# Kernel optimization log

Hardware: AMD Instinct MI355X
Metric: run time of the kernel (lower is better)

The kernel has to match this reference:

```python
import jax, jax.numpy as jnp
import numpy as np
from jax import lax

S, B, H, V = 1024, 32, 512, 32000  # seq_len, batch, hidden, vocab


def setup_inputs() -> dict:
    key = jax.random.key(0)
    ks = jax.random.split(key, 12)
    d = {"word_inputs": jax.random.randint(ks[0], (S, B), 0, V)}
    d["embedding"] = jax.random.normal(ks[1], (V, H), jnp.float32) * 0.02
    s = 1.0 / np.sqrt(H)
    i = 2
    for n in ["fwd1", "fwd2", "bwd1", "bwd2"]:
        d[f"W_ih_{n}"] = jax.random.uniform(ks[i], (4 * H, H), jnp.float32, -s, s); i += 1
        d[f"W_hh_{n}"] = jax.random.uniform(ks[i], (4 * H, H), jnp.float32, -s, s); i += 1
        d[f"b_ih_{n}"] = jnp.zeros((4 * H,), jnp.float32)
        d[f"b_hh_{n}"] = jnp.zeros((4 * H,), jnp.float32)
    return d


def _lstm_step(x, h, c, W_ih, W_hh, b, mask):
    # torch.nn.LSTMCell gate order: i, f, g, o
    g = x @ W_ih.T + h @ W_hh.T + b  # [B, 4H]
    i_, f_, g_, o_ = jnp.split(g, 4, axis=-1)
    c_new = jax.nn.sigmoid(f_) * c + jax.nn.sigmoid(i_) * jnp.tanh(g_)
    h_new = jax.nn.sigmoid(o_) * jnp.tanh(c_new)
    m = mask[:, None]  # mask True => keep old state (padding step)
    return jnp.where(m, h, h_new), jnp.where(m, c, c_new)


def _run_direction(emb, masks, p1, p2):
    z = jnp.zeros((emb.shape[1], p1[0].shape[0] // 4), emb.dtype)

    def step(carry, xm):
        h1, c1, h2, c2 = carry
        x, m = xm
        h1, c1 = _lstm_step(x, h1, c1, p1[0], p1[1], p1[2], m)
        h2, c2 = _lstm_step(h1, h2, c2, p2[0], p2[1], p2[2], m)
        return (h1, c1, h2, c2), h2

    carry, hs = lax.scan(step, (z, z, z, z), (emb, masks))
    return hs, carry


def reference(word_inputs, embedding,
              W_ih_fwd1, W_hh_fwd1, b_ih_fwd1, b_hh_fwd1,
              W_ih_fwd2, W_hh_fwd2, b_ih_fwd2, b_hh_fwd2,
              W_ih_bwd1, W_hh_bwd1, b_ih_bwd1, b_hh_bwd1,
              W_ih_bwd2, W_hh_bwd2, b_ih_bwd2, b_hh_bwd2):
    # dropout in eval mode (identity) for a deterministic reference
    emb = embedding[word_inputs]           # [S, B, H]
    masks = word_inputs == 1               # padding token id == 1
    p_f1 = (W_ih_fwd1, W_hh_fwd1, b_ih_fwd1 + b_hh_fwd1)
    p_f2 = (W_ih_fwd2, W_hh_fwd2, b_ih_fwd2 + b_hh_fwd2)
    p_b1 = (W_ih_bwd1, W_hh_bwd1, b_ih_bwd1 + b_hh_bwd1)
    p_b2 = (W_ih_bwd2, W_hh_bwd2, b_ih_bwd2 + b_hh_bwd2)
    fhs, _ = _run_direction(emb, masks, p_f1, p_f2)
    bhs, bcarry = _run_direction(emb[::-1], masks[::-1], p_b1, p_b2)
    # original: outputs[i] = fhs[i] + reversed(bhs)[i] / 2  (note: only bwd halved)
    outputs = fhs + bhs[::-1] / 2
    bh1, bc1, bh2, bc2 = bcarry  # final backward states (bstatus1, bstatus2)
    return outputs, bh1, bc1, bh2, bc2
```

## Files before the change

### kernel.cpp

```cpp
#include <hip/hip_runtime.h>
#include <math.h>


#define SEQ 1024
#define NB 32
#define NH 512
#define BH (NB*NH)
#define NV 32000
#define KP 1032

typedef __attribute__((ext_vector_type(8))) short short8;
typedef __attribute__((ext_vector_type(4))) float f32x4;
typedef unsigned long long u64;

struct P {
  const int*   word;
  const float* emb;
  const float* Wih[4];
  const float* Whh[4];
  const float* bih[4];
  const float* bhh[4];
  unsigned* flags;
  unsigned* gen;
  unsigned short* hpk;
  const unsigned* embP;
  float* out;
  float* bwd;
};

__device__ __forceinline__ unsigned short f2bf(float x) {
  unsigned u = __float_as_uint(x);
  return (unsigned short)((u + 0x7fffu + ((u >> 16) & 1u)) >> 16);
}
__device__ __forceinline__ float bf2f(unsigned short b) {
  return __uint_as_float(((unsigned)b) << 16);
}
__device__ __forceinline__ float sigf(float x) { return 1.0f / (1.0f + expf(-x)); }

__device__ __forceinline__ unsigned ald(const unsigned* p_) {
  return __hip_atomic_load((unsigned*)p_, __ATOMIC_RELAXED, __HIP_MEMORY_SCOPE_AGENT);
}
__device__ __forceinline__ u64 ald64(const u64* p_) {
  return __hip_atomic_load((u64*)p_, __ATOMIC_RELAXED, __HIP_MEMORY_SCOPE_AGENT);
}
__device__ __forceinline__ void ast(unsigned* p_, unsigned v) {
  __hip_atomic_store(p_, v, __ATOMIC_RELAXED, __HIP_MEMORY_SCOPE_AGENT);
}
__device__ __forceinline__ void ast16(unsigned short* p_, unsigned short v) {
  __hip_atomic_store(p_, v, __ATOMIC_RELAXED, __HIP_MEMORY_SCOPE_AGENT);
}
__device__ __forceinline__ float aldf(const float* p_) {
  return __hip_atomic_load((float*)p_, __ATOMIC_RELAXED, __HIP_MEMORY_SCOPE_AGENT);
}
__device__ __forceinline__ void astf(float* p_, float v) {
  __hip_atomic_store(p_, v, __ATOMIC_RELAXED, __HIP_MEMORY_SCOPE_AGENT);
}

__device__ __forceinline__ void stage_slab16(const unsigned short* slab,
                                             unsigned short* xhHi,
                                             int Lpair, int koff) {
  const u64* s64 = (const u64*)slab;
  u64 A[16];
#pragma unroll
  for (int q = 0; q < 16; ++q) A[q] = ald64(s64 + Lpair + q * 128);
#pragma unroll
  for (int q = 0; q < 16; ++q) {
    const int idx = Lpair + q * 128;
    const int r   = idx >> 7;
    const int uc  = (idx & 127) * 4;
    *(u64*)(xhHi + r * KP + koff + uc) = A[q];
  }
}

__global__ void conv_embp(const float* __restrict__ e,
                          unsigned* __restrict__ pk) {
  const size_t i = ((size_t)blockIdx.x * 256 + threadIdx.x) * 8;
  float4 a = *(const float4*)(e + i);
  float4 b = *(const float4*)(e + i + 4);
  float xs[8] = {a.x, a.y, a.z, a.w, b.x, b.y, b.z, b.w};
  unsigned o[8];
#pragma unroll
  for (int q = 0; q < 8; ++q) {
    unsigned short hb = f2bf(xs[q]);
    unsigned short lb = f2bf(xs[q] - bf2f(hb));
    o[q] = (unsigned)hb | ((unsigned)lb << 16);
  }
  uint4 v0, v1;
  v0.x=o[0]; v0.y=o[1]; v0.z=o[2]; v0.w=o[3];
  v1.x=o[4]; v1.y=o[5]; v1.z=o[6]; v1.w=o[7];
  *(uint4*)(pk + i)     = v0;
  *(uint4*)(pk + i + 4) = v1;
}

__global__ void merge_out(float* __restrict__ out, const float* __restrict__ bwd) {
  const size_t i = ((size_t)blockIdx.x * 256 + threadIdx.x) * 4;
  float4 a = *(const float4*)(out + i);
  const float4 b = *(const float4*)(bwd + i);
  a.x += b.x; a.y += b.y; a.z += b.z; a.w += b.w;
  *(float4*)(out + i) = a;
}

__global__ __launch_bounds__(256, 1) void enc_persist(P p) {
  extern __shared__ unsigned short smem[];
  unsigned short* xhHi = smem;
  unsigned short* xhLo = smem + 16 * KP;
  float* gl2 = (float*)(smem + 32 * KP);

  const int tid  = threadIdx.x;
  const int bid  = blockIdx.x;
  const int dl   = bid >> 6;
  const int dir  = dl >> 1, layer = dl & 1;
  const int r6   = bid & 63;
  const int u0   = (r6 >> 1) * 16;
  const int b0   = (r6 & 1) * 16;
  const int lane = tid & 63, wv = tid >> 6;

  const int dom  = p.bwd ? (dir * 2 + (r6 & 1)) : 0;
  const int lid  = p.bwd ? (layer * 32 + (r6 >> 1)) : bid;

  const bool use_lo = (layer == 0) && (wv < 2);

  short8 aHi[32], aLo[32];
  {
    const int kg = (lane >> 4) * 8;
#pragma unroll
    for (int gg = 0; gg < 4; ++gg) {
      const int gr = gg * 512 + u0 + (lane & 15);
      const float* Wi = p.Wih[dl] + (size_t)gr * NH;
      const float* Wh = p.Whh[dl] + (size_t)gr * NH;
#pragma unroll
      for (int kk = 0; kk < 8; ++kk) {
        const int k0 = (wv * 8 + kk) * 32 + kg;
        const float* s = (k0 < 512) ? (Wi + k0) : (Wh + (k0 - 512));
        float4 v0 = *(const float4*)s;
        float4 v1 = *(const float4*)(s + 4);
        float xs[8] = {v0.x, v0.y, v0.z, v0.w, v1.x, v1.y, v1.z, v1.w};
        short8 h8, l8;
#pragma unroll
        for (int q = 0; q < 8; ++q) {
          unsigned short hb = f2bf(xs[q]);
          h8[q] = (short)hb;
          l8[q] = (short)f2bf(xs[q] - bf2f(hb));
        }
        aHi[gg * 8 + kk] = h8; aLo[gg * 8 + kk] = l8;
      }
    }
  }

  const int cu = tid & 15, cb = tid >> 4;
  const int uG = u0 + cu;
  const float bi  = p.bih[dl][uG]        + p.bhh[dl][uG];
  const float bf_ = p.bih[dl][512 + uG]  + p.bhh[dl][512 + uG];
  const float bg  = p.bih[dl][1024 + uG] + p.bhh[dl][1024 + uG];
  const float bo  = p.bih[dl][1536 + uG] + p.bhh[dl][1536 + uG];

  float c_reg = 0.f, h_reg = 0.f;

  const int sr = tid >> 4;
  const int rb = tid & 15;
  const int ks = sr * 64;

  const int rp = tid >> 3;
  const int lp = tid & 7;

  int tk, tk_st, tk_pk;
  {
    const int to0 = dir ? (SEQ - 1) : 0;
    tk    = p.word[(size_t)to0 * NB + b0 + cb];
    tk_st = p.word[(size_t)to0 * NB + b0 + rb];
    tk_pk = p.word[(size_t)to0 * NB + b0 + (rp & 15)];
  }

  const bool use_pk = (layer == 0) && (tid < 128) && (p.embP != nullptr);
  const bool do_epf = (layer == 0) && (sr < 8) && (p.embP == nullptr);
  union { float4 f[16]; uint4 u[16]; } epr;
  if (use_pk) {
    const uint4* src = (const uint4*)(p.embP + (size_t)tk_pk * NH);
#pragma unroll
    for (int q = 0; q < 16; ++q) epr.u[q] = src[lp + q * 8];
  } else if (do_epf) {
    const float* e = p.emb + (size_t)tk_st * NH + ks;
#pragma unroll
    for (int q = 0; q < 16; ++q) epr.f[q] = *(const float4*)(e + q * 4);
  }

  for (int j = 0; j <= SEQ; ++j) {
    const int act = layer ? (j >= 1) : (j < SEQ);
    const int t = layer ? (j - 1) : j;
    const int torig = dir ? (SEQ - 1 - t) : t;
    const int par = j & 1;

    float out_v = 0.f;
    float* out_tgt = nullptr;

    if (act) {
      if (wv < 2) {
        if (layer == 0) {
          if (p.embP) {
#pragma unroll
            for (int q = 0; q < 16; ++q) {
              const uint4 w = epr.u[q];
              const int u = 4 * (lp + q * 8);
              uint2 hv, lv;
              hv.x = (w.x & 0xffffu) | (w.y << 16);
              hv.y = (w.z & 0xffffu) | (w.w << 16);
              lv.x = (w.x >> 16)     | (w.y & 0xffff0000u);
              lv.y = (w.z >> 16)     | (w.w & 0xffff0000u);
              *(uint2*)(xhHi + rp * KP + u) = hv;
              *(uint2*)(xhLo + rp * KP + u) = lv;
            }
          } else {
#pragma unroll
            for (int h2 = 0; h2 < 2; ++h2) {
#pragma unroll
              for (int q = 0; q < 4; ++q) {
                const float4 va = epr.f[h2 * 8 + 2 * q];
                const float4 vb = epr.f[h2 * 8 + 2 * q + 1];
                float xs[8] = {va.x, va.y, va.z, va.w, vb.x, vb.y, vb.z, vb.w};
                unsigned hw[4], lw[4];
#pragma unroll
                for (int m = 0; m < 4; ++m) {
                  unsigned short ha = f2bf(xs[2*m]);
                  unsigned short hc = f2bf(xs[2*m+1]);
                  unsigned short la = f2bf(xs[2*m]   - bf2f(ha));
                  unsigned short lc = f2bf(xs[2*m+1] - bf2f(hc));
                  hw[m] = (unsigned)ha | ((unsigned)hc << 16);
                  lw[m] = (unsigned)la | ((unsigned)lc << 16);
                }
                uint4 hv, lv;
                hv.x=hw[0]; hv.y=hw[1]; hv.z=hw[2]; hv.w=hw[3];
                lv.x=lw[0]; lv.y=lw[1]; lv.z=lw[2]; lv.w=lw[3];
                *(uint4*)(xhHi + rb * KP + ks + h2 * 32 + q * 8) = hv;
                *(uint4*)(xhLo + rb * KP + ks + h2 * 32 + q * 8) = lv;
              }
            }
          }
        } else {
          const unsigned short* slab = p.hpk + (size_t)((dl - 1) * 2 + par) * BH
                                             + (size_t)b0 * NH;
          stage_slab16(slab, xhHi, tid, 0);
        }
      } else {
        const unsigned short* slab = p.hpk + (size_t)(dl * 2 + par) * BH
                                           + (size_t)b0 * NH;
        stage_slab16(slab, xhHi, tid - 128, 512);
      }
    }

    int tk_nx = tk, tk_st_nx = tk_st, tk_pk_nx = tk_pk;
    if (j < SEQ) {
      int t_nx = layer ? j : (j + 1);
      if (t_nx > SEQ - 1) t_nx = SEQ - 1;
      const int to_nx = dir ? (SEQ - 1 - t_nx) : t_nx;
      tk_nx    = p.word[(size_t)to_nx * NB + b0 + cb];
      tk_st_nx = p.word[(size_t)to_nx * NB + b0 + rb];
      tk_pk_nx = p.word[(size_t)to_nx * NB + b0 + (rp & 15)];
    }

    float out_pf = 0.f;
    size_t oi = 0;
    int do_add = 0;
    if (act && layer == 1) {
      oi = (size_t)torig * BH + (size_t)(b0 + cb) * NH + uG;
      if (!p.bwd) {
        do_add = dir ? (torig < 512) : (torig > 511);
        if (do_add) out_pf = aldf(p.out + oi);
      }
    }

    __syncthreads();

    if (act) {
      f32x4 aA[4], aBC[4];
#pragma unroll
      for (int gg = 0; gg < 4; ++gg) {
        aA[gg]  = (f32x4){0.f, 0.f, 0.f, 0.f};
        aBC[gg] = (f32x4){0.f, 0.f, 0.f, 0.f};
      }
      const unsigned short* bp = xhHi + (lane & 15) * KP + (lane >> 4) * 8;
      const unsigned short* bq = xhLo + (lane & 15) * KP + (lane >> 4) * 8;
#pragma unroll
      for (int kk = 0; kk < 8; ++kk) {
        const int kc = wv * 8 + kk;
        short8 bH = *(const short8*)(bp + kc * 32);
#pragma unroll
        for (int gg = 0; gg < 4; ++gg) {
          aA[gg]  = __builtin_amdgcn_mfma_f32_16x16x32_bf16(aHi[gg*8+kk], bH, aA[gg],  0, 0, 0);
          aBC[gg] = __builtin_amdgcn_mfma_f32_16x16x32_bf16(aLo[gg*8+kk], bH, aBC[gg], 0, 0, 0);
        }
        if (use_lo) {
          short8 bL = *(const short8*)(bq + kc * 32);
#pragma unroll
          for (int gg = 0; gg < 4; ++gg)
            aBC[gg] = __builtin_amdgcn_mfma_f32_16x16x32_bf16(aHi[gg*8+kk], bL, aBC[gg], 0, 0, 0);
        }
      }
#pragma unroll
      for (int gg = 0; gg < 4; ++gg) {
        f32x4 acc = aA[gg] + aBC[gg];
        *(f32x4*)&gl2[((wv * 4 + gg) * 16 + (lane & 15)) * 20 + (lane >> 4) * 4] = acc;
      }
    }
    __syncthreads();

    if (act) {
#define GL2(w_,g_) gl2[(((w_) * 4 + (g_)) * 16 + cb) * 20 + cu]
      const float vi = ((GL2(0,0)+GL2(1,0)) + (GL2(2,0)+GL2(3,0))) + bi;
      const float vf = ((GL2(0,1)+GL2(1,1)) + (GL2(2,1)+GL2(3,1))) + bf_;
      const float vg = ((GL2(0,2)+GL2(1,2)) + (GL2(2,2)+GL2(3,2))) + bg;
      const float vo = ((GL2(0,3)+GL2(1,3)) + (GL2(2,3)+GL2(3,3))) + bo;
#undef GL2
      float cn = sigf(vf) * c_reg + sigf(vi) * tanhf(vg);
      float hn = sigf(vo) * tanhf(cn);
      if (tk == 1) { cn = c_reg; hn = h_reg; }
      c_reg = cn; h_reg = hn;
      const size_t hix = (size_t)(dl * 2 + (par ^ 1)) * BH + (size_t)(b0 + cb) * NH + uG;
      ast16(p.hpk + hix, f2bf(hn));
      if (layer == 1) {
        if (p.bwd) {
          out_v = dir ? (0.5f * hn) : hn;
          out_tgt = (dir ? p.bwd : p.out) + oi;
        } else {
          const float v = dir ? (0.5f * hn) : hn;
          astf(p.out + oi, do_add ? (out_pf + v) : v);
        }
      }
    }

    tk = tk_nx; tk_st = tk_st_nx; tk_pk = tk_pk_nx;

    __syncthreads();
    if (tid == 0)
      ast(p.flags + (size_t)(dom * 64 + lid) * 16, (unsigned)(j + 1));

    if (out_tgt) astf(out_tgt, out_v);

    if (j + 1 < SEQ) {
      if (use_pk) {
        const uint4* src = (const uint4*)(p.embP + (size_t)tk_pk * NH);
#pragma unroll
        for (int q = 0; q < 16; ++q) epr.u[q] = src[lp + q * 8];
      } else if (do_epf) {
        const float* e = p.emb + (size_t)tk_st * NH + ks;
#pragma unroll
        for (int q = 0; q < 16; ++q) epr.f[q] = *(const float4*)(e + q * 4);
      }
    }

    if (p.bwd) {
      if (tid < 64) {
        unsigned* f = p.flags + (size_t)(dom * 64 + tid) * 16;
        while (ald(f) < (unsigned)(j + 1)) __builtin_amdgcn_s_sleep(1);
      }
      __syncthreads();
    } else {
      if (bid == 0) {
        unsigned* f = p.flags + (size_t)tid * 16;
        while (ald(f) < (unsigned)(j + 1)) __builtin_amdgcn_s_sleep(1);
        __syncthreads();
        if (tid == 0) ast(p.gen, (unsigned)(j + 1));
      } else {
        if (tid < 64) {
          while (ald(p.gen) < (unsigned)(j + 1)) __builtin_amdgcn_s_sleep(1);
        }
        __syncthreads();
      }
    }
  }

  if (dl == 2) {
    p.out[(size_t)SEQ * BH + 0 * (size_t)BH + (size_t)(b0 + cb) * NH + uG] = h_reg;
    p.out[(size_t)SEQ * BH + 1 * (size_t)BH + (size_t)(b0 + cb) * NH + uG] = c_reg;
  } else if (dl == 3) {
    p.out[(size_t)SEQ * BH + 2 * (size_t)BH + (size_t)(b0 + cb) * NH + uG] = h_reg;
    p.out[(size_t)SEQ * BH + 3 * (size_t)BH + (size_t)(b0 + cb) * NH + uG] = c_reg;
  }
}

extern "C" void kernel_launch(void* const* d_in, const int* in_sizes, int n_in,
                              void* d_out, int out_size, void* d_ws, size_t ws_size,
                              hipStream_t stream) {
  P p;
  p.word = (const int*)d_in[0];
  p.emb  = (const float*)d_in[1];
  for (int i = 0; i < 4; ++i) {
    p.Wih[i] = (const float*)d_in[2 + i * 4 + 0];
    p.Whh[i] = (const float*)d_in[2 + i * 4 + 1];
    p.bih[i] = (const float*)d_in[2 + i * 4 + 2];
    p.bhh[i] = (const float*)d_in[2 + i * 4 + 3];
  }
  unsigned char* ws = (unsigned char*)d_ws;
  p.flags = (unsigned*)ws;
  p.gen   = (unsigned*)(ws + 16384);
  p.hpk   = (unsigned short*)(ws + 16896);
  const size_t embOff   = (size_t)1 << 20;
  const size_t embBytes = (size_t)NV * NH * 4;
  p.embP = (ws_size >= embOff + embBytes) ? (const unsigned*)(ws + embOff)
                                          : nullptr;
  const size_t bwdOff   = (size_t)65 << 20;
  const size_t bwdBytes = (size_t)SEQ * BH * 4;
  const bool split = (ws_size >= bwdOff + bwdBytes) && (p.embP != nullptr);
  p.bwd = split ? (float*)(ws + bwdOff) : nullptr;
  p.out = (float*)d_out;

  hipMemsetAsync(d_ws, 0, 16896 + (size_t)8 * BH * 2, stream);

  if (p.embP) {
    hipLaunchKernelGGL(conv_embp, dim3(8000), dim3(256), 0, stream,
                       p.emb, (unsigned*)p.embP);
  }

  const int smem = 90112;
  hipFuncSetAttribute(reinterpret_cast<const void*>(enc_persist),
                      hipFuncAttributeMaxDynamicSharedMemorySize, smem);
  hipLaunchKernelGGL(enc_persist, dim3(256), dim3(256), smem, stream, p);

  if (split) {
    hipLaunchKernelGGL(merge_out, dim3(16384), dim3(256), 0, stream,
                       p.out, p.bwd);
  }
}
```

Before: 3.898 ms.

## Load MFMA B fragments directly from global in bwd path, skipping LDS staging

In the split-domain (p.bwd) path, each wave now loads its MFMA B operands straight into registers. It reads embedding hi/lo fragments from the packed embedding buffer, and recurrent h fragments from the hpk slabs through atomic 64-bit loads. This removes the LDS staging writes and the __syncthreads that used to come before the MFMA loop. It cuts one block-wide barrier and the LDS round trip per timestep on the latency-critical recurrence, at the cost of more registers and uncoalesced global loads.

```diff
diff --git a/kernel.cpp b/kernel.cpp
--- a/kernel.cpp
+++ b/kernel.cpp
@@ -119,6 +119,7 @@
   const int lid  = p.bwd ? (layer * 32 + (r6 >> 1)) : bid;
 
   const bool use_lo = (layer == 0) && (wv < 2);
+  const bool frag_emb = use_lo && (p.bwd != nullptr) && (p.embP != nullptr);
 
   short8 aHi[32], aLo[32];
   {
@@ -159,22 +160,30 @@
   const int sr = tid >> 4;
   const int rb = tid & 15;
   const int ks = sr * 64;
-
   const int rp = tid >> 3;
   const int lp = tid & 7;
 
-  int tk, tk_st, tk_pk;
+  const int n    = lane & 15;
+  const int kg16 = (lane >> 4) * 8;
+
+  int tk, tk_st, tk_pk, tk_fr;
   {
     const int to0 = dir ? (SEQ - 1) : 0;
     tk    = p.word[(size_t)to0 * NB + b0 + cb];
     tk_st = p.word[(size_t)to0 * NB + b0 + rb];
     tk_pk = p.word[(size_t)to0 * NB + b0 + (rp & 15)];
-  }
-
-  const bool use_pk = (layer == 0) && (tid < 128) && (p.embP != nullptr);
+    tk_fr = p.word[(size_t)to0 * NB + b0 + n];
+  }
+
+  const bool use_pk = (layer == 0) && (tid < 128) && (p.embP != nullptr) && !p.bwd;
   const bool do_epf = (layer == 0) && (sr < 8) && (p.embP == nullptr);
   union { float4 f[16]; uint4 u[16]; } epr;
-  if (use_pk) {
+  if (frag_emb) {
+    const unsigned* src = p.embP + (size_t)tk_fr * NH + (wv * 8) * 32 + kg16;
+#pragma unroll
+    for (int q = 0; q < 16; ++q)
+      epr.u[q] = *(const uint4*)(src + (q >> 1) * 32 + (q & 1) * 4);
+  } else if (use_pk) {
     const uint4* src = (const uint4*)(p.embP + (size_t)tk_pk * NH);
 #pragma unroll
     for (int q = 0; q < 16; ++q) epr.u[q] = src[lp + q * 8];
@@ -193,7 +202,26 @@
     float out_v = 0.f;
     float* out_tgt = nullptr;
 
-    if (act) {
+    u64 B64[16];
+    if (p.bwd) {
+      if (act && !frag_emb) {
+        const unsigned short* slab;
+        int kbase;
+        if (wv < 2) {
+          slab = p.hpk + (size_t)((dl - 1) * 2 + par) * BH + (size_t)b0 * NH;
+          kbase = wv * 8;
+        } else {
+          slab = p.hpk + (size_t)(dl * 2 + par) * BH + (size_t)b0 * NH;
+          kbase = (wv - 2) * 8;
+        }
+#pragma unroll
+        for (int kk = 0; kk < 8; ++kk) {
+          const unsigned short* a = slab + (size_t)n * NH + (kbase + kk) * 32 + kg16;
+          B64[2 * kk]     = ald64((const u64*)a);
+          B64[2 * kk + 1] = ald64((const u64*)a + 1);
+        }
+      }
+    } else if (act) {
       if (wv < 2) {
         if (layer == 0) {
           if (p.embP) {
@@ -247,7 +275,7 @@
       }
     }
 
-    int tk_nx = tk, tk_st_nx = tk_st, tk_pk_nx = tk_pk;
+    int tk_nx = tk, tk_st_nx = tk_st, tk_pk_nx = tk_pk, tk_fr_nx = tk_fr;
     if (j < SEQ) {
       int t_nx = layer ? j : (j + 1);
       if (t_nx > SEQ - 1) t_nx = SEQ - 1;
@@ -255,6 +283,7 @@
       tk_nx    = p.word[(size_t)to_nx * NB + b0 + cb];
       tk_st_nx = p.word[(size_t)to_nx * NB + b0 + rb];
       tk_pk_nx = p.word[(size_t)to_nx * NB + b0 + (rp & 15)];
+      tk_fr_nx = p.word[(size_t)to_nx * NB + b0 + n];
     }
 
     float out_pf = 0.f;
@@ -268,7 +297,7 @@
       }
     }
 
-    __syncthreads();
+    if (!p.bwd) __syncthreads();
 
     if (act) {
       f32x4 aA[4], aBC[4];
@@ -282,14 +311,31 @@
 #pragma unroll
       for (int kk = 0; kk < 8; ++kk) {
         const int kc = wv * 8 + kk;
-        short8 bH = *(const short8*)(bp + kc * 32);
+        short8 bH, bL;
+        if (p.bwd) {
+          if (frag_emb) {
+            const uint4 w0 = epr.u[2 * kk], w1 = epr.u[2 * kk + 1];
+            const unsigned ww[8] = {w0.x, w0.y, w0.z, w0.w, w1.x, w1.y, w1.z, w1.w};
+#pragma unroll
+            for (int e = 0; e < 8; ++e) {
+              bH[e] = (short)(ww[e] & 0xffffu);
+              bL[e] = (short)(ww[e] >> 16);
+            }
+          } else {
+            union { u64 v[2]; short8 s; } cv;
+            cv.v[0] = B64[2 * kk]; cv.v[1] = B64[2 * kk + 1];
+            bH = cv.s;
+          }
+        } else {
+          bH = *(const short8*)(bp + kc * 32);
+          if (use_lo) bL = *(const short8*)(bq + kc * 32);
+        }
 #pragma unroll
         for (int gg = 0; gg < 4; ++gg) {
           aA[gg]  = __builtin_amdgcn_mfma_f32_16x16x32_bf16(aHi[gg*8+kk], bH, aA[gg],  0, 0, 0);
           aBC[gg] = __builtin_amdgcn_mfma_f32_16x16x32_bf16(aLo[gg*8+kk], bH, aBC[gg], 0, 0, 0);
         }
         if (use_lo) {
-          short8 bL = *(const short8*)(bq + kc * 32);
 #pragma unroll
           for (int gg = 0; gg < 4; ++gg)
             aBC[gg] = __builtin_amdgcn_mfma_f32_16x16x32_bf16(aHi[gg*8+kk], bL, aBC[gg], 0, 0, 0);
@@ -327,7 +373,7 @@
       }
     }
 
-    tk = tk_nx; tk_st = tk_st_nx; tk_pk = tk_pk_nx;
+    tk = tk_nx; tk_st = tk_st_nx; tk_pk = tk_pk_nx; tk_fr = tk_fr_nx;
 
     __syncthreads();
     if (tid == 0)
@@ -336,7 +382,12 @@
     if (out_tgt) astf(out_tgt, out_v);
 
     if (j + 1 < SEQ) {
-      if (use_pk) {
+      if (frag_emb) {
+        const unsigned* src = p.embP + (size_t)tk_fr * NH + (wv * 8) * 32 + kg16;
+#pragma unroll
+        for (int q = 0; q < 16; ++q)
+          epr.u[q] = *(const uint4*)(src + (q >> 1) * 32 + (q & 1) * 4);
+      } else if (use_pk) {
         const uint4* src = (const uint4*)(p.embP + (size_t)tk_pk * NH);
 #pragma unroll
         for (int q = 0; q < 16; ++q) epr.u[q] = src[lp + q * 8];
```

New measurement: 4.732 ms. +21.4%, slower.
